# Optimization experiments

Hardware: AMD Instinct MI355X
Metric: run time of the kernel (lower is better)

The kernel has to match this reference:

```python
import jax, jax.numpy as jnp
import numpy as np

L = 4096            # lattice side (L_num)
R = 4.8             # public-goods enhancement factor r
GAMMA = 0.8         # discount
EPSILON = 0.02      # exploration rate
ETA = 0.8           # Q-learning mixing rate (self.eta)
NEG_BIG = 1.0e9


def neigh5(x):
    # 3x3 cross kernel conv on wrap-padded grid == circular 5-point sum
    return (x + jnp.roll(x, 1, 0) + jnp.roll(x, -1, 0)
              + jnp.roll(x, 1, 1) + jnp.roll(x, -1, 1))


def setup_inputs() -> dict:
    key = jax.random.key(0)
    k1, k2, k3, k4, k5 = jax.random.split(key, 5)
    N = L * L
    type_t_matrix = jax.random.randint(k1, (L, L), 0, 2, dtype=jnp.int32)
    # q_table ~ 0.5*randn + [2.0, 1.5] offset on next-state axis (as in __init__)
    offs = jnp.array([2.0, 1.5], dtype=jnp.float32)
    q_table = jax.random.normal(k2, (N, 2, 2), dtype=jnp.float32) * 0.5 + offs[None, None, :]
    rand_tensor = jax.random.uniform(k3, (N, 2), dtype=jnp.float32)
    random_type = jax.random.randint(k4, (L, L), 0, 2, dtype=jnp.int32)
    epsilon_rand = jax.random.uniform(k5, (L, L), dtype=jnp.float32)
    return {"type_t_matrix": type_t_matrix, "q_table": q_table,
            "rand_tensor": rand_tensor, "random_type": random_type,
            "epsilon_rand": epsilon_rand}


def reference(type_t_matrix, q_table, rand_tensor, random_type, epsilon_rand):
    N = L * L
    # --- calculation_value: profit on toroidal lattice ---
    c = (type_t_matrix == 1).astype(jnp.float32)  # cooperators
    d = (type_t_matrix == 0).astype(jnp.float32)  # defectors
    coop_num = neigh5(c)                          # cooperators in 5-neighborhood
    c_profit = coop_num / 5.0 * R - 1.0
    d_profit = coop_num / 5.0 * R
    profit = neigh5(c_profit) * c + neigh5(d_profit) * d  # (L, L)

    # --- type_matrix_change: epsilon-greedy action selection ---
    A = type_t_matrix.reshape(-1)                 # current state per cell (N,)
    C = jnp.arange(N)
    Qp = q_table[C, A]                            # (N, 2) action values
    maxv = jnp.max(Qp, axis=1, keepdims=True)
    max_t = (Qp == maxv).astype(jnp.float32)      # argmax mask (ties)
    masked = max_t - (1.0 - max_t) * NEG_BIG
    greedy = jnp.argmax(masked + rand_tensor, axis=1)  # random tie-break
    explore_mask = (epsilon_rand >= EPSILON).reshape(-1)
    B = jnp.where(explore_mask, greedy.astype(jnp.int32), random_type.reshape(-1))

    # --- updateQMatrix: indexed gather/scatter Q update ---
    max_values = jnp.max(q_table[C, B], axis=1)   # max_a' Q[s', a']
    upd = (1.0 - ETA) * q_table[C, A, B] + ETA * (profit.reshape(-1) + GAMMA * max_values)
    q_new = q_table.at[C, A, B].set(upd)

    type_t1_matrix = B.reshape(L, L).astype(jnp.float32)
    return type_t1_matrix, q_new, profit
```

## Files before the change

### kernel.cpp

```cpp
#include <hip/hip_runtime.h>

#define L 4096
#define LMASK 4095
#define NCELL (L * L)

typedef float f32x2 __attribute__((ext_vector_type(2)));

__global__ __launch_bounds__(256) void spgg_qlearn_kernel(
    const int*    __restrict__ type_t,
    const float4* __restrict__ qtab,
    const float*  __restrict__ rnd,
    const int*    __restrict__ rtype,
    const float*  __restrict__ eps,
    float*        __restrict__ out_type,
    float4*       __restrict__ out_q,
    float*        __restrict__ out_profit)
{
    const int i = blockIdx.x * 256 + threadIdx.x;
    const int r = i >> 12;
    const int c = i & LMASK;

    const int r0  = r << 12;
    const int rm1 = ((r - 1) & LMASK) << 12;
    const int rp1 = ((r + 1) & LMASK) << 12;
    const int rm2 = ((r - 2) & LMASK) << 12;
    const int rp2 = ((r + 2) & LMASK) << 12;
    const int cm1 = (c - 1) & LMASK;
    const int cp1 = (c + 1) & LMASK;
    const int cm2 = (c - 2) & LMASK;
    const int cp2 = (c + 2) & LMASK;

    const int t00 = type_t[r0 + c];
    const int f1  = type_t[rm2 + c];
    const int f2  = type_t[rp2 + c];
    const int f3  = type_t[r0 + cm2];
    const int f4  = type_t[r0 + cp2];
    const int x1  = type_t[rm1 + c];
    const int x2  = type_t[rp1 + c];
    const int x3  = type_t[r0 + cm1];
    const int x4  = type_t[r0 + cp1];
    const int g1  = type_t[rm1 + cm1];
    const int g2  = type_t[rm1 + cp1];
    const int g3  = type_t[rp1 + cm1];
    const int g4  = type_t[rp1 + cp1];

    float4 q = qtab[i];
    const float e = eps[i];
    const int  rt = rtype[i];

    const int w13 = 5 * t00 + 2 * (x1 + x2 + x3 + x4) + 2 * (g1 + g2 + g3 + g4)
                  + (f1 + f2 + f3 + f4);

    const float profit = 0.96f * (float)w13 - 5.0f * (float)t00;

    const int A = t00;
    const float qa0 = A ? q.z : q.x;
    const float qa1 = A ? q.w : q.y;

    int greedy = (qa1 > qa0) ? 1 : 0;

    if (__any(qa0 == qa1)) {
        f32x2 rv;
        asm volatile("global_load_dwordx2 %0, %1, off\n\t"
                     "s_waitcnt vmcnt(0)"
                     : "=v"(rv) : "v"(rnd + 2 * (long)i));
        if (qa0 == qa1) greedy = (rv.y > rv.x) ? 1 : 0;
    }

    const int B = (e >= 0.02f) ? greedy : rt;

    const float qb0 = B ? q.z : q.x;
    const float qb1 = B ? q.w : q.y;
    const float maxv = fmaxf(qb0, qb1);

    const int ab = A * 2 + B;
    const float qab = (ab == 0) ? q.x : (ab == 1) ? q.y : (ab == 2) ? q.z : q.w;
    const float upd = 0.2f * qab + 0.8f * (profit + 0.8f * maxv);

    q.x = (ab == 0) ? upd : q.x;
    q.y = (ab == 1) ? upd : q.y;
    q.z = (ab == 2) ? upd : q.z;
    q.w = (ab == 3) ? upd : q.w;

    out_type[i]   = (float)B;
    out_q[i]      = q;
    out_profit[i] = profit;
}

extern "C" void kernel_launch(void* const* d_in, const int* in_sizes, int n_in,
                              void* d_out, int out_size, void* d_ws, size_t ws_size,
                              hipStream_t stream) {
    const int*    type_t = (const int*)d_in[0];
    const float4* qtab   = (const float4*)d_in[1];
    const float*  rnd    = (const float*)d_in[2];
    const int*    rtype  = (const int*)d_in[3];
    const float*  eps    = (const float*)d_in[4];

    float* out    = (float*)d_out;
    float* o_type = out;
    float4* o_q   = (float4*)(out + NCELL);
    float* o_prof = out + 5 * (size_t)NCELL;

    spgg_qlearn_kernel<<<NCELL / 256, 256, 0, stream>>>(
        type_t, qtab, rnd, rtype, eps, o_type, o_q, o_prof);
}
```

Before: 160.7 us.

## Process four cells per thread with vectorized stencil and I/O loads

Each thread now handles four consecutive cells, loading the type grid as int4 vectors (11 vector loads instead of 13 scalar loads per cell) and reusing neighbors across the four cells in registers. Eps, random_type, type and profit outputs move to 128-bit accesses, and the block size drops to 128 threads. This cuts load instruction count and redundant neighbor fetches. The cost is more registers per thread and fewer threads in flight, and the Q-table accesses become strided per thread instead of coalesced across the wavefront.

```diff
diff --git a/kernel.cpp b/kernel.cpp
--- a/kernel.cpp
+++ b/kernel.cpp
@@ -5,102 +5,140 @@
 #define NCELL (L * L)
 
 typedef float f32x2 __attribute__((ext_vector_type(2)));
+typedef float f32x4 __attribute__((ext_vector_type(4)));
+typedef int   i32x4 __attribute__((ext_vector_type(4)));
 
-__global__ __launch_bounds__(256) void spgg_qlearn_kernel(
-    const int*    __restrict__ type_t,
-    const float4* __restrict__ qtab,
-    const float*  __restrict__ rnd,
-    const int*    __restrict__ rtype,
-    const float*  __restrict__ eps,
-    float*        __restrict__ out_type,
-    float4*       __restrict__ out_q,
-    float*        __restrict__ out_profit)
+#define QSEL(qv, Aj, gj, tj)                                   \
+    {   const float qa0_ = (Aj) ? qv.z : qv.x;                 \
+        const float qa1_ = (Aj) ? qv.w : qv.y;                 \
+        gj = (qa1_ > qa0_) ? 1 : 0;                            \
+        tj = (qa0_ == qa1_); }
+
+#define QUPD(qv, Aj, ej, rtj, profj, gj, Bj)                   \
+    {   const int B_ = ((ej) >= 0.02f) ? (gj) : (rtj);         \
+        const float mx_ = B_ ? fmaxf(qv.z, qv.w)               \
+                             : fmaxf(qv.x, qv.y);              \
+        const int ab_ = (Aj) * 2 + B_;                         \
+        const float qab_ = (ab_ == 0) ? qv.x : (ab_ == 1) ? qv.y \
+                         : (ab_ == 2) ? qv.z : qv.w;           \
+        const float u_ = 0.2f * qab_ + 0.8f * ((profj) + 0.8f * mx_); \
+        qv.x = (ab_ == 0) ? u_ : qv.x;                         \
+        qv.y = (ab_ == 1) ? u_ : qv.y;                         \
+        qv.z = (ab_ == 2) ? u_ : qv.z;                         \
+        qv.w = (ab_ == 3) ? u_ : qv.w;                         \
+        Bj = B_; }
+
+__global__ __launch_bounds__(128) void spgg_qlearn_kernel(
+    const int*   __restrict__ type_t,
+    const f32x4* __restrict__ qtab,
+    const float* __restrict__ rnd,
+    const i32x4* __restrict__ rtype4,
+    const f32x4* __restrict__ eps4,
+    f32x4*       __restrict__ out_type4,
+    f32x4*       __restrict__ out_q,
+    f32x4*       __restrict__ out_prof4)
 {
-    const int i = blockIdx.x * 256 + threadIdx.x;
-    const int r = i >> 12;
-    const int c = i & LMASK;
+    const i32x4* __restrict__ T4 = (const i32x4*)type_t;
 
-    const int r0  = r << 12;
-    const int rm1 = ((r - 1) & LMASK) << 12;
-    const int rp1 = ((r + 1) & LMASK) << 12;
-    const int rm2 = ((r - 2) & LMASK) << 12;
-    const int rp2 = ((r + 2) & LMASK) << 12;
-    const int cm1 = (c - 1) & LMASK;
-    const int cp1 = (c + 1) & LMASK;
-    const int cm2 = (c - 2) & LMASK;
-    const int cp2 = (c + 2) & LMASK;
+    const int g  = blockIdx.x * 128 + threadIdx.x;
+    const int i0 = g << 2;
+    const int r  = i0 >> 12;
+    const int c0 = i0 & LMASK;
 
-    const int t00 = type_t[r0 + c];
-    const int f1  = type_t[rm2 + c];
-    const int f2  = type_t[rp2 + c];
-    const int f3  = type_t[r0 + cm2];
-    const int f4  = type_t[r0 + cp2];
-    const int x1  = type_t[rm1 + c];
-    const int x2  = type_t[rp1 + c];
-    const int x3  = type_t[r0 + cm1];
-    const int x4  = type_t[r0 + cp1];
-    const int g1  = type_t[rm1 + cm1];
-    const int g2  = type_t[rm1 + cp1];
-    const int g3  = type_t[rp1 + cm1];
-    const int g4  = type_t[rp1 + cp1];
+    const int R0  = r << 10;
+    const int Rm1 = ((r - 1) & LMASK) << 10;
+    const int Rp1 = ((r + 1) & LMASK) << 10;
+    const int Rm2 = ((r - 2) & LMASK) << 10;
+    const int Rp2 = ((r + 2) & LMASK) << 10;
+    const int Pc  = c0 >> 2;
+    const int Pm  = ((c0 - 4) & LMASK) >> 2;
+    const int Pp  = ((c0 + 4) & LMASK) >> 2;
 
-    float4 q = qtab[i];
-    const float e = eps[i];
-    const int  rt = rtype[i];
+    const i32x4 rA = T4[R0 + Pm],  rB = T4[R0 + Pc],  rC = T4[R0 + Pp];
+    const i32x4 mA = T4[Rm1 + Pm], mB = T4[Rm1 + Pc], mC = T4[Rm1 + Pp];
+    const i32x4 pA = T4[Rp1 + Pm], pB = T4[Rp1 + Pc], pC = T4[Rp1 + Pp];
+    const i32x4 m2 = T4[Rm2 + Pc], p2 = T4[Rp2 + Pc];
 
-    const int w13 = 5 * t00 + 2 * (x1 + x2 + x3 + x4) + 2 * (g1 + g2 + g3 + g4)
-                  + (f1 + f2 + f3 + f4);
+    f32x4 q0 = qtab[i0];
+    f32x4 q1 = qtab[i0 + 1];
+    f32x4 q2 = qtab[i0 + 2];
+    f32x4 q3 = qtab[i0 + 3];
+    const f32x4 e4 = eps4[g];
+    const i32x4 rt = rtype4[g];
 
-    const float profit = 0.96f * (float)w13 - 5.0f * (float)t00;
+    const int rowr[12] = {rA.x,rA.y,rA.z,rA.w, rB.x,rB.y,rB.z,rB.w, rC.x,rC.y,rC.z,rC.w};
+    const int rowm[12] = {mA.x,mA.y,mA.z,mA.w, mB.x,mB.y,mB.z,mB.w, mC.x,mC.y,mC.z,mC.w};
+    const int rowp[12] = {pA.x,pA.y,pA.z,pA.w, pB.x,pB.y,pB.z,pB.w, pC.x,pC.y,pC.z,pC.w};
+    const int rm2_[4]  = {m2.x, m2.y, m2.z, m2.w};
+    const int rp2_[4]  = {p2.x, p2.y, p2.z, p2.w};
 
-    const int A = t00;
-    const float qa0 = A ? q.z : q.x;
-    const float qa1 = A ? q.w : q.y;
-
-    int greedy = (qa1 > qa0) ? 1 : 0;
-
-    if (__any(qa0 == qa1)) {
-        f32x2 rv;
-        asm volatile("global_load_dwordx2 %0, %1, off\n\t"
-                     "s_waitcnt vmcnt(0)"
-                     : "=v"(rv) : "v"(rnd + 2 * (long)i));
-        if (qa0 == qa1) greedy = (rv.y > rv.x) ? 1 : 0;
+    float prof[4];
+    int   Aa[4];
+    #pragma unroll
+    for (int j = 0; j < 4; ++j) {
+        const int jj = j + 4;
+        const int self = rowr[jj];
+        const int w = 5 * self
+            + 2 * (rowr[jj-1] + rowr[jj+1] + rowm[jj] + rowp[jj]
+                 + rowm[jj-1] + rowm[jj+1] + rowp[jj-1] + rowp[jj+1])
+            + (rowr[jj-2] + rowr[jj+2] + rm2_[j] + rp2_[j]);
+        prof[j] = 0.96f * (float)w - 5.0f * (float)self;
+        Aa[j] = self;
     }
 
-    const int B = (e >= 0.02f) ? greedy : rt;
+    int g0, g1, g2, g3;
+    bool t0, t1, t2, t3;
+    QSEL(q0, Aa[0], g0, t0)
+    QSEL(q1, Aa[1], g1, t1)
+    QSEL(q2, Aa[2], g2, t2)
+    QSEL(q3, Aa[3], g3, t3)
 
-    const float qb0 = B ? q.z : q.x;
-    const float qb1 = B ? q.w : q.y;
-    const float maxv = fmaxf(qb0, qb1);
+    if (__any(t0 || t1 || t2 || t3)) {
+        f32x2 v0, v1, v2, v3;
+        asm volatile("global_load_dwordx2 %0, %4, off\n\t"
+                     "global_load_dwordx2 %1, %5, off\n\t"
+                     "global_load_dwordx2 %2, %6, off\n\t"
+                     "global_load_dwordx2 %3, %7, off\n\t"
+                     "s_waitcnt vmcnt(0)"
+                     : "=v"(v0), "=v"(v1), "=v"(v2), "=v"(v3)
+                     : "v"(rnd + 2 * (long)i0),     "v"(rnd + 2 * (long)i0 + 2),
+                       "v"(rnd + 2 * (long)i0 + 4), "v"(rnd + 2 * (long)i0 + 6));
+        if (t0) g0 = (v0.y > v0.x) ? 1 : 0;
+        if (t1) g1 = (v1.y > v1.x) ? 1 : 0;
+        if (t2) g2 = (v2.y > v2.x) ? 1 : 0;
+        if (t3) g3 = (v3.y > v3.x) ? 1 : 0;
+    }
 
-    const int ab = A * 2 + B;
-    const float qab = (ab == 0) ? q.x : (ab == 1) ? q.y : (ab == 2) ? q.z : q.w;
-    const float upd = 0.2f * qab + 0.8f * (profit + 0.8f * maxv);
+    int B0, B1, B2, B3;
+    QUPD(q0, Aa[0], e4.x, rt.x, prof[0], g0, B0)
+    QUPD(q1, Aa[1], e4.y, rt.y, prof[1], g1, B1)
+    QUPD(q2, Aa[2], e4.z, rt.z, prof[2], g2, B2)
+    QUPD(q3, Aa[3], e4.w, rt.w, prof[3], g3, B3)
 
-    q.x = (ab == 0) ? upd : q.x;
-    q.y = (ab == 1) ? upd : q.y;
-    q.z = (ab == 2) ? upd : q.z;
-    q.w = (ab == 3) ? upd : q.w;
-
-    out_type[i]   = (float)B;
-    out_q[i]      = q;
-    out_profit[i] = profit;
+    f32x4 ot; ot.x = (float)B0; ot.y = (float)B1; ot.z = (float)B2; ot.w = (float)B3;
+    f32x4 pf; pf.x = prof[0];   pf.y = prof[1];   pf.z = prof[2];   pf.w = prof[3];
+    out_q[i0]     = q0;
+    out_q[i0 + 1] = q1;
+    out_q[i0 + 2] = q2;
+    out_q[i0 + 3] = q3;
+    out_type4[g]  = ot;
+    out_prof4[g]  = pf;
 }
 
 extern "C" void kernel_launch(void* const* d_in, const int* in_sizes, int n_in,
                               void* d_out, int out_size, void* d_ws, size_t ws_size,
                               hipStream_t stream) {
-    const int*    type_t = (const int*)d_in[0];
-    const float4* qtab   = (const float4*)d_in[1];
-    const float*  rnd    = (const float*)d_in[2];
-    const int*    rtype  = (const int*)d_in[3];
-    const float*  eps    = (const float*)d_in[4];
+    const int*   type_t = (const int*)d_in[0];
+    const f32x4* qtab   = (const f32x4*)d_in[1];
+    const float* rnd    = (const float*)d_in[2];
+    const i32x4* rtype4 = (const i32x4*)d_in[3];
+    const f32x4* eps4   = (const f32x4*)d_in[4];
 
-    float* out    = (float*)d_out;
-    float* o_type = out;
-    float4* o_q   = (float4*)(out + NCELL);
-    float* o_prof = out + 5 * (size_t)NCELL;
+    float* out       = (float*)d_out;
+    f32x4* o_type4   = (f32x4*)out;
+    f32x4* o_q       = (f32x4*)(out + NCELL);
+    f32x4* o_prof4   = (f32x4*)(out + 5 * (size_t)NCELL);
 
-    spgg_qlearn_kernel<<<NCELL / 256, 256, 0, stream>>>(
-        type_t, qtab, rnd, rtype, eps, o_type, o_q, o_prof);
+    spgg_qlearn_kernel<<<NCELL / 512, 128, 0, stream>>>(
+        type_t, qtab, rnd, rtype4, eps4, o_type4, o_q, o_prof4);
 }
```

New measurement: 185.0 us. 1.15x slower.
